# Kernel tuning notes

Hardware: AMD Instinct MI355X
Metric: run time of the kernel (lower is better)

Reference implementation:

```python
import jax, jax.numpy as jnp
import numpy as np

EPS = 1e-12  # torch F.normalize eps


def _pairwise_unit_diffs(x):
    # x: [B, N, D] -> unit-normalized pairwise diffs [B, N*N, D]
    B, N, D = x.shape
    d = x[:, :, None, :] - x[:, None, :, :]            # [B, N, N, D]
    n = jnp.linalg.norm(d, axis=-1, keepdims=True)
    d = d / jnp.maximum(n, EPS)                        # zero rows stay zero
    return d.reshape(B, N * N, D)


def setup_inputs() -> dict:
    key = jax.random.key(0)
    k1, k2 = jax.random.split(key)
    B, N, D = 4, 64, 128
    student = jax.random.normal(k1, (B, N, D), dtype=jnp.float32)
    teacher = jax.random.normal(k2, (B, N, D), dtype=jnp.float32)
    return {"student": student, "teacher": teacher}


def reference(student, teacher):
    B, N, D = student.shape
    sd = _pairwise_unit_diffs(student)                              # [B, N^2, D]
    td = jax.lax.stop_gradient(_pairwise_unit_diffs(teacher))      # [B, N^2, D]
    s_ang = jnp.einsum('bkd,bld->bkl', sd, sd)
    t_ang = jax.lax.stop_gradient(jnp.einsum('bkd,bld->bkl', td, td))
    # smooth L1 (beta=1.0), summed then divided by total element count
    diff = s_ang - t_ang
    ad = jnp.abs(diff)
    loss = jnp.where(ad < 1.0, 0.5 * diff * diff, ad - 0.5)
    count = B * (N * N) * (N * N)
    return jnp.sum(loss) / count
```

## Files before the change

### kernel.cpp

```cpp
#include <hip/hip_runtime.h>


#define EPSF 1e-12f

typedef __bf16 bf16x8 __attribute__((ext_vector_type(8)));
typedef float  f32x4  __attribute__((ext_vector_type(4)));

__device__ __forceinline__ float rinv_from_nsq(float nsq)
{
    float n = sqrtf(fmaxf(nsq, 0.0f));
    return 1.0f / fmaxf(n, EPSF);
}

__device__ __forceinline__ void cvt8(float4 u, float4 v, bf16x8& h, bf16x8& l)
{
    float uu[8] = {u.x, u.y, u.z, u.w, v.x, v.y, v.z, v.w};
#pragma unroll
    for (int i = 0; i < 8; ++i) {
        __bf16 hh = (__bf16)uu[i];
        h[i] = hh;
        l[i] = (__bf16)(uu[i] - (float)hh);
    }
}

__global__ __launch_bounds__(512) void fused_kernel(
    const float* __restrict__ student, const float* __restrict__ teacher,
    float* __restrict__ out)
{
    __shared__ float Gs[4096];
    __shared__ float Gt[4096];
    __shared__ __align__(16) float pool[17408];
    __shared__ float red[8];

    int b   = blockIdx.x / 63;
    int kc  = blockIdx.x % 63;
    int tid = threadIdx.x;

    {
        int r  = tid >> 3;
        int f8 = tid & 7;
        const float* Xs = student + b * 8192 + r * 128 + f8 * 16;
        const float* Xt = teacher + b * 8192 + r * 128 + f8 * 16;
        float* sHi = pool + 0 * 4352 + r * 68 + f8 * 8;
        float* sLo = pool + 1 * 4352 + r * 68 + f8 * 8;
        float* tHi = pool + 2 * 4352 + r * 68 + f8 * 8;
        float* tLo = pool + 3 * 4352 + r * 68 + f8 * 8;
#pragma unroll
        for (int c = 0; c < 2; ++c) {
            float4 u = *(const float4*)(Xs + c * 8);
            float4 v = *(const float4*)(Xs + c * 8 + 4);
            bf16x8 h, l;
            cvt8(u, v, h, l);
            *(bf16x8*)(sHi + c * 4) = h;
            *(bf16x8*)(sLo + c * 4) = l;
            u = *(const float4*)(Xt + c * 8);
            v = *(const float4*)(Xt + c * 8 + 4);
            cvt8(u, v, h, l);
            *(bf16x8*)(tHi + c * 4) = h;
            *(bf16x8*)(tLo + c * 4) = l;
        }
    }
    __syncthreads();

    {
        int wid  = tid >> 6;
        int lane = tid & 63;
        int l15  = lane & 15;
        int quad = lane >> 4;
        int tensor = wid >> 2;
        int mt     = wid & 3;
        const float* XH = pool + tensor * 8704;
        const float* XL = XH + 4352;

        bf16x8 aH[4], aL[4];
        int abase = (mt * 16 + l15) * 68 + quad * 4;
#pragma unroll
        for (int ks = 0; ks < 4; ++ks) {
            aH[ks] = *(const bf16x8*)(XH + abase + ks * 16);
            aL[ks] = *(const bf16x8*)(XL + abase + ks * 16);
        }
        float* Gd = tensor ? Gt : Gs;
#pragma unroll
        for (int nt = 0; nt < 4; ++nt) {
            f32x4 acc = {0.f, 0.f, 0.f, 0.f};
            int bbase = (nt * 16 + l15) * 68 + quad * 4;
#pragma unroll
            for (int ks = 0; ks < 4; ++ks) {
                bf16x8 bH = *(const bf16x8*)(XH + bbase + ks * 16);
                bf16x8 bL = *(const bf16x8*)(XL + bbase + ks * 16);
                acc = __builtin_amdgcn_mfma_f32_16x16x32_bf16(aH[ks], bH, acc, 0, 0, 0);
                acc = __builtin_amdgcn_mfma_f32_16x16x32_bf16(aH[ks], bL, acc, 0, 0, 0);
                acc = __builtin_amdgcn_mfma_f32_16x16x32_bf16(aL[ks], bH, acc, 0, 0, 0);
                acc = __builtin_amdgcn_mfma_f32_16x16x32_bf16(aL[ks], bL, acc, 0, 0, 0);
            }
#pragma unroll
            for (int reg = 0; reg < 4; ++reg)
                Gd[(mt * 16 + quad * 4 + reg) * 64 + nt * 16 + l15] = acc[reg];
        }
    }
    __syncthreads();

    float* vs = pool;
    float* vt = pool + 2176;

    {
        int m  = tid >> 4;
        int q4 = (tid & 15) * 4;
        int t  = kc * 32 + m;
        int i = 0, rem = t;
        while (rem >= 63 - i) { rem -= 63 - i; ++i; }
        int j = i + 1 + rem;

        float rsij = rinv_from_nsq(Gs[i * 65] - 2.f * Gs[i * 64 + j] + Gs[j * 65]);
        float rtij = rinv_from_nsq(Gt[i * 65] - 2.f * Gt[i * 64 + j] + Gt[j * 65]);

        float4 gis = *(const float4*)(Gs + i * 64 + q4);
        float4 gjs = *(const float4*)(Gs + j * 64 + q4);
        float4 git = *(const float4*)(Gt + i * 64 + q4);
        float4 gjt = *(const float4*)(Gt + j * 64 + q4);
        float4 v;
        v.x = (gis.x - gjs.x) * rsij;
        v.y = (gis.y - gjs.y) * rsij;
        v.z = (gis.z - gjs.z) * rsij;
        v.w = (gis.w - gjs.w) * rsij;
        *(float4*)(vs + m * 68 + q4) = v;
        v.x = (git.x - gjt.x) * rtij;
        v.y = (git.y - gjt.y) * rtij;
        v.z = (git.z - gjt.z) * rtij;
        v.w = (git.w - gjt.w) * rtij;
        *(float4*)(vt + m * 68 + q4) = v;
    }

    int msub = tid >> 7;
    int pos  = tid & 127;
    int pg = 0, qg = 0;
    float4 rsv[4], rtv[4];
    if (pos < 120) {
        int rem = pos;
        while (rem >= 15 - pg) { rem -= 15 - pg; ++pg; }
        qg = pg + 1 + rem;
        int p4  = pg * 4;
        float dps[4], dpt[4];
#pragma unroll
        for (int cc = 0; cc < 4; ++cc) {
            dps[cc] = Gs[(p4 + cc) * 65];
            dpt[cc] = Gt[(p4 + cc) * 65];
        }
#pragma unroll
        for (int k = 0; k < 4; ++k) {
            int q = qg * 4 + k;
            float4 g = *(const float4*)(Gs + q * 64 + p4);
            float gqq = Gs[q * 65];
            rsv[k].x = rinv_from_nsq(dps[0] - 2.f * g.x + gqq);
            rsv[k].y = rinv_from_nsq(dps[1] - 2.f * g.y + gqq);
            rsv[k].z = rinv_from_nsq(dps[2] - 2.f * g.z + gqq);
            rsv[k].w = rinv_from_nsq(dps[3] - 2.f * g.w + gqq);
            float4 hh = *(const float4*)(Gt + q * 64 + p4);
            float hqq = Gt[q * 65];
            rtv[k].x = rinv_from_nsq(dpt[0] - 2.f * hh.x + hqq);
            rtv[k].y = rinv_from_nsq(dpt[1] - 2.f * hh.y + hqq);
            rtv[k].z = rinv_from_nsq(dpt[2] - 2.f * hh.z + hqq);
            rtv[k].w = rinv_from_nsq(dpt[3] - 2.f * hh.w + hqq);
        }
    }
    __syncthreads();

    float ac0 = 0.f, ac1 = 0.f, ac2 = 0.f, ac3 = 0.f;

#define SL1(acc, spc, sqc, tpc, tqc, rsk, rtk)                                  \
    {                                                                           \
        float d  = (spc - sqc) * rsk - (tpc - tqc) * rtk;                       \
        float a  = fabsf(d);                                                    \
        float mn = fminf(a, 1.0f);                                              \
        acc = fmaf(mn, fmaf(-0.5f, mn, a), acc);                                \
    }

    if (pos < 120) {
        int p4  = pg * 4;
        int q4l = qg * 4;
#pragma unroll 4
        for (int mm = 0; mm < 8; ++mm) {
            int m = mm * 4 + msub;
            const float* vsm = vs + m * 68;
            const float* vtm = vt + m * 68;
            float4 sp = *(const float4*)(vsm + p4);
            float4 tp = *(const float4*)(vtm + p4);
            float4 sq = *(const float4*)(vsm + q4l);
            float4 tq = *(const float4*)(vtm + q4l);

            SL1(ac0, sp.x, sq.x, tp.x, tq.x, rsv[0].x, rtv[0].x)
            SL1(ac0, sp.y, sq.x, tp.y, tq.x, rsv[0].y, rtv[0].y)
            SL1(ac0, sp.z, sq.x, tp.z, tq.x, rsv[0].z, rtv[0].z)
            SL1(ac0, sp.w, sq.x, tp.w, tq.x, rsv[0].w, rtv[0].w)

            SL1(ac1, sp.x, sq.y, tp.x, tq.y, rsv[1].x, rtv[1].x)
            SL1(ac1, sp.y, sq.y, tp.y, tq.y, rsv[1].y, rtv[1].y)
            SL1(ac1, sp.z, sq.y, tp.z, tq.y, rsv[1].z, rtv[1].z)
            SL1(ac1, sp.w, sq.y, tp.w, tq.y, rsv[1].w, rtv[1].w)

            SL1(ac2, sp.x, sq.z, tp.x, tq.z, rsv[2].x, rtv[2].x)
            SL1(ac2, sp.y, sq.z, tp.y, tq.z, rsv[2].y, rtv[2].y)
            SL1(ac2, sp.z, sq.z, tp.z, tq.z, rsv[2].z, rtv[2].z)
            SL1(ac2, sp.w, sq.z, tp.w, tq.z, rsv[2].w, rtv[2].w)

            SL1(ac3, sp.x, sq.w, tp.x, tq.w, rsv[3].x, rtv[3].x)
            SL1(ac3, sp.y, sq.w, tp.y, tq.w, rsv[3].y, rtv[3].y)
            SL1(ac3, sp.z, sq.w, tp.z, tq.w, rsv[3].z, rtv[3].z)
            SL1(ac3, sp.w, sq.w, tp.w, tq.w, rsv[3].w, rtv[3].w)
        }
    }

    {
        int m  = tid >> 4;
        int g4 = (tid & 15) * 4;
        float4 s4 = *(const float4*)(vs + m * 68 + g4);
        float4 t4 = *(const float4*)(vt + m * 68 + g4);

        float d0s = Gs[(g4 + 0) * 65], d1s = Gs[(g4 + 1) * 65];
        float d2s = Gs[(g4 + 2) * 65], d3s = Gs[(g4 + 3) * 65];
        float d0t = Gt[(g4 + 0) * 65], d1t = Gt[(g4 + 1) * 65];
        float d2t = Gt[(g4 + 2) * 65], d3t = Gt[(g4 + 3) * 65];

        float rs01 = rinv_from_nsq(d0s - 2.f * Gs[(g4 + 0) * 64 + g4 + 1] + d1s);
        float rs02 = rinv_from_nsq(d0s - 2.f * Gs[(g4 + 0) * 64 + g4 + 2] + d2s);
        float rs03 = rinv_from_nsq(d0s - 2.f * Gs[(g4 + 0) * 64 + g4 + 3] + d3s);
        float rs12 = rinv_from_nsq(d1s - 2.f * Gs[(g4 + 1) * 64 + g4 + 2] + d2s);
        float rs13 = rinv_from_nsq(d1s - 2.f * Gs[(g4 + 1) * 64 + g4 + 3] + d3s);
        float rs23 = rinv_from_nsq(d2s - 2.f * Gs[(g4 + 2) * 64 + g4 + 3] + d3s);
        float rt01 = rinv_from_nsq(d0t - 2.f * Gt[(g4 + 0) * 64 + g4 + 1] + d1t);
        float rt02 = rinv_from_nsq(d0t - 2.f * Gt[(g4 + 0) * 64 + g4 + 2] + d2t);
        float rt03 = rinv_from_nsq(d0t - 2.f * Gt[(g4 + 0) * 64 + g4 + 3] + d3t);
        float rt12 = rinv_from_nsq(d1t - 2.f * Gt[(g4 + 1) * 64 + g4 + 2] + d2t);
        float rt13 = rinv_from_nsq(d1t - 2.f * Gt[(g4 + 1) * 64 + g4 + 3] + d3t);
        float rt23 = rinv_from_nsq(d2t - 2.f * Gt[(g4 + 2) * 64 + g4 + 3] + d3t);

        SL1(ac0, s4.x, s4.y, t4.x, t4.y, rs01, rt01)
        SL1(ac1, s4.x, s4.z, t4.x, t4.z, rs02, rt02)
        SL1(ac2, s4.x, s4.w, t4.x, t4.w, rs03, rt03)
        SL1(ac3, s4.y, s4.z, t4.y, t4.z, rs12, rt12)
        SL1(ac0, s4.y, s4.w, t4.y, t4.w, rs13, rt13)
        SL1(ac1, s4.z, s4.w, t4.z, t4.w, rs23, rt23)
    }
#undef SL1

    float acc = (ac0 + ac1) + (ac2 + ac3);

    for (int off = 32; off > 0; off >>= 1)
        acc += __shfl_down(acc, off);
    int lane = tid & 63;
    int wave = tid >> 6;
    if (lane == 0) red[wave] = acc;
    __syncthreads();
    if (tid < 8) {
        float v = red[tid];
        v += __shfl_down(v, 4);
        v += __shfl_down(v, 2);
        v += __shfl_down(v, 1);
        if (tid == 0) atomicAdd(out, v * (1.0f / 16777216.0f));
    }
}

extern "C" void kernel_launch(void* const* d_in, const int* in_sizes, int n_in,
                              void* d_out, int out_size, void* d_ws, size_t ws_size,
                              hipStream_t stream)
{
    const float* student = (const float*)d_in[0];
    const float* teacher = (const float*)d_in[1];
    (void)d_ws; (void)ws_size;
    fused_kernel<<<252, 512, 0, stream>>>(student, teacher, (float*)d_out);
}
```

Baseline: 68.91 us.

## Double block size, precompute inverse pair norms table in LDS, closed-form pair indexing

Raises the block to 1024 threads and spreads every phase (load/convert, MFMA Gram, vector build, SL1 loop) across twice as many waves. Adds a shared-memory table of reciprocal pairwise distance norms, built once with the hardware rsq instruction, so the later stages read it instead of recomputing sqrt and divide many times. Replaces the serial while-loops that map a linear index to a triangular (i,j) pair with a closed-form sqrt formula plus a correction step. The gain in parallelism comes with an extra barrier, heavier register pressure under the 1024-thread launch bound, and slightly different rounding from rsq.

```diff
diff --git a/kernel.cpp b/kernel.cpp
--- a/kernel.cpp
+++ b/kernel.cpp
@@ -1,15 +1,14 @@
 #include <hip/hip_runtime.h>
 
 
-#define EPSF 1e-12f
+#define EPSQ 1e-24f
 
 typedef __bf16 bf16x8 __attribute__((ext_vector_type(8)));
 typedef float  f32x4  __attribute__((ext_vector_type(4)));
 
-__device__ __forceinline__ float rinv_from_nsq(float nsq)
-{
-    float n = sqrtf(fmaxf(nsq, 0.0f));
-    return 1.0f / fmaxf(n, EPSF);
+__device__ __forceinline__ float rinv_nsq(float nsq)
+{
+    return __builtin_amdgcn_rsqf(fmaxf(nsq, EPSQ));
 }
 
 __device__ __forceinline__ void cvt8(float4 u, float4 v, bf16x8& h, bf16x8& l)
@@ -23,42 +22,39 @@
     }
 }
 
-__global__ __launch_bounds__(512) void fused_kernel(
+__global__ __launch_bounds__(1024) void fused_kernel(
     const float* __restrict__ student, const float* __restrict__ teacher,
     float* __restrict__ out)
 {
     __shared__ float Gs[4096];
     __shared__ float Gt[4096];
     __shared__ __align__(16) float pool[17408];
-    __shared__ float red[8];
+    __shared__ float red[16];
 
     int b   = blockIdx.x / 63;
     int kc  = blockIdx.x % 63;
     int tid = threadIdx.x;
 
     {
-        int r  = tid >> 3;
-        int f8 = tid & 7;
-        const float* Xs = student + b * 8192 + r * 128 + f8 * 16;
-        const float* Xt = teacher + b * 8192 + r * 128 + f8 * 16;
-        float* sHi = pool + 0 * 4352 + r * 68 + f8 * 8;
-        float* sLo = pool + 1 * 4352 + r * 68 + f8 * 8;
-        float* tHi = pool + 2 * 4352 + r * 68 + f8 * 8;
-        float* tLo = pool + 3 * 4352 + r * 68 + f8 * 8;
-#pragma unroll
-        for (int c = 0; c < 2; ++c) {
-            float4 u = *(const float4*)(Xs + c * 8);
-            float4 v = *(const float4*)(Xs + c * 8 + 4);
-            bf16x8 h, l;
-            cvt8(u, v, h, l);
-            *(bf16x8*)(sHi + c * 4) = h;
-            *(bf16x8*)(sLo + c * 4) = l;
-            u = *(const float4*)(Xt + c * 8);
-            v = *(const float4*)(Xt + c * 8 + 4);
-            cvt8(u, v, h, l);
-            *(bf16x8*)(tHi + c * 4) = h;
-            *(bf16x8*)(tLo + c * 4) = l;
-        }
+        int r = tid >> 4;
+        int h = tid & 15;
+        const float* Xs = student + b * 8192 + r * 128 + h * 8;
+        const float* Xt = teacher + b * 8192 + r * 128 + h * 8;
+        float* sHi = pool + 0 * 4352 + r * 68 + h * 4;
+        float* sLo = pool + 1 * 4352 + r * 68 + h * 4;
+        float* tHi = pool + 2 * 4352 + r * 68 + h * 4;
+        float* tLo = pool + 3 * 4352 + r * 68 + h * 4;
+        float4 u = *(const float4*)(Xs);
+        float4 v = *(const float4*)(Xs + 4);
+        bf16x8 hh, ll;
+        cvt8(u, v, hh, ll);
+        *(bf16x8*)sHi = hh;
+        *(bf16x8*)sLo = ll;
+        u = *(const float4*)(Xt);
+        v = *(const float4*)(Xt + 4);
+        cvt8(u, v, hh, ll);
+        *(bf16x8*)tHi = hh;
+        *(bf16x8*)tLo = ll;
     }
     __syncthreads();
 
@@ -67,8 +63,10 @@
         int lane = tid & 63;
         int l15  = lane & 15;
         int quad = lane >> 4;
-        int tensor = wid >> 2;
-        int mt     = wid & 3;
+        int tensor = wid >> 3;
+        int w8     = wid & 7;
+        int mt     = w8 >> 1;
+        int nh     = w8 & 1;
         const float* XH = pool + tensor * 8704;
         const float* XL = XH + 4352;
 
@@ -81,7 +79,8 @@
         }
         float* Gd = tensor ? Gt : Gs;
 #pragma unroll
-        for (int nt = 0; nt < 4; ++nt) {
+        for (int nn = 0; nn < 2; ++nn) {
+            int nt = nh * 2 + nn;
             f32x4 acc = {0.f, 0.f, 0.f, 0.f};
             int bbase = (nt * 16 + l15) * 68 + quad * 4;
 #pragma unroll
@@ -100,35 +99,58 @@
     }
     __syncthreads();
 
-    float* vs = pool;
-    float* vt = pool + 2176;
-
-    {
-        int m  = tid >> 4;
-        int q4 = (tid & 15) * 4;
+    float* vs  = pool;
+    float* vt  = pool + 2176;
+    float* rnS = pool + 4352;
+    float* rnT = pool + 8448;
+
+    {
+        int tensor = tid >> 9;
+        int u      = tid & 511;
+        int p      = u >> 3;
+        int q0     = (u & 7) * 8;
+        const float* Gd = tensor ? Gt : Gs;
+        float*       rn = tensor ? rnT : rnS;
+        float dp = Gd[p * 65];
+        float4 g0 = *(const float4*)(Gd + p * 64 + q0);
+        float4 g1 = *(const float4*)(Gd + p * 64 + q0 + 4);
+        float4 o0, o1;
+        o0.x = rinv_nsq(dp - 2.f * g0.x + Gd[(q0 + 0) * 65]);
+        o0.y = rinv_nsq(dp - 2.f * g0.y + Gd[(q0 + 1) * 65]);
+        o0.z = rinv_nsq(dp - 2.f * g0.z + Gd[(q0 + 2) * 65]);
+        o0.w = rinv_nsq(dp - 2.f * g0.w + Gd[(q0 + 3) * 65]);
+        o1.x = rinv_nsq(dp - 2.f * g1.x + Gd[(q0 + 4) * 65]);
+        o1.y = rinv_nsq(dp - 2.f * g1.y + Gd[(q0 + 5) * 65]);
+        o1.z = rinv_nsq(dp - 2.f * g1.z + Gd[(q0 + 6) * 65]);
+        o1.w = rinv_nsq(dp - 2.f * g1.w + Gd[(q0 + 7) * 65]);
+        *(float4*)(rn + p * 64 + q0)     = o0;
+        *(float4*)(rn + p * 64 + q0 + 4) = o1;
+    }
+    __syncthreads();
+
+    {
+        int m  = tid >> 5;
+        int qh = (tid & 31) * 2;
         int t  = kc * 32 + m;
-        int i = 0, rem = t;
-        while (rem >= 63 - i) { rem -= 63 - i; ++i; }
-        int j = i + 1 + rem;
-
-        float rsij = rinv_from_nsq(Gs[i * 65] - 2.f * Gs[i * 64 + j] + Gs[j * 65]);
-        float rtij = rinv_from_nsq(Gt[i * 65] - 2.f * Gt[i * 64 + j] + Gt[j * 65]);
-
-        float4 gis = *(const float4*)(Gs + i * 64 + q4);
-        float4 gjs = *(const float4*)(Gs + j * 64 + q4);
-        float4 git = *(const float4*)(Gt + i * 64 + q4);
-        float4 gjt = *(const float4*)(Gt + j * 64 + q4);
-        float4 v;
-        v.x = (gis.x - gjs.x) * rsij;
-        v.y = (gis.y - gjs.y) * rsij;
-        v.z = (gis.z - gjs.z) * rsij;
-        v.w = (gis.w - gjs.w) * rsij;
-        *(float4*)(vs + m * 68 + q4) = v;
-        v.x = (git.x - gjt.x) * rtij;
-        v.y = (git.y - gjt.y) * rtij;
-        v.z = (git.z - gjt.z) * rtij;
-        v.w = (git.w - gjt.w) * rtij;
-        *(float4*)(vt + m * 68 + q4) = v;
+        int i = (int)(0.5f * (127.0f - sqrtf((float)(16129 - 8 * t))));
+        if (i * (127 - i) / 2 > t) --i;
+        else if ((i + 1) * (126 - i) / 2 <= t) ++i;
+        int j = i + 1 + (t - i * (127 - i) / 2);
+
+        float rsij = rnS[i * 64 + j];
+        float rtij = rnT[i * 64 + j];
+
+        float2 gi = *(const float2*)(Gs + i * 64 + qh);
+        float2 gj = *(const float2*)(Gs + j * 64 + qh);
+        float2 o;
+        o.x = (gi.x - gj.x) * rsij;
+        o.y = (gi.y - gj.y) * rsij;
+        *(float2*)(vs + m * 68 + qh) = o;
+        gi = *(const float2*)(Gt + i * 64 + qh);
+        gj = *(const float2*)(Gt + j * 64 + qh);
+        o.x = (gi.x - gj.x) * rtij;
+        o.y = (gi.y - gj.y) * rtij;
+        *(float2*)(vt + m * 68 + qh) = o;
     }
 
     int msub = tid >> 7;
@@ -136,31 +158,15 @@
     int pg = 0, qg = 0;
     float4 rsv[4], rtv[4];
     if (pos < 120) {
-        int rem = pos;
-        while (rem >= 15 - pg) { rem -= 15 - pg; ++pg; }
-        qg = pg + 1 + rem;
-        int p4  = pg * 4;
-        float dps[4], dpt[4];
-#pragma unroll
-        for (int cc = 0; cc < 4; ++cc) {
-            dps[cc] = Gs[(p4 + cc) * 65];
-            dpt[cc] = Gt[(p4 + cc) * 65];
-        }
+        pg = (int)(0.5f * (31.0f - sqrtf((float)(961 - 8 * pos))));
+        if (pg * (31 - pg) / 2 > pos) --pg;
+        else if ((pg + 1) * (30 - pg) / 2 <= pos) ++pg;
+        qg = pg + 1 + (pos - pg * (31 - pg) / 2);
+        int p4 = pg * 4;
 #pragma unroll
         for (int k = 0; k < 4; ++k) {
-            int q = qg * 4 + k;
-            float4 g = *(const float4*)(Gs + q * 64 + p4);
-            float gqq = Gs[q * 65];
-            rsv[k].x = rinv_from_nsq(dps[0] - 2.f * g.x + gqq);
-            rsv[k].y = rinv_from_nsq(dps[1] - 2.f * g.y + gqq);
-            rsv[k].z = rinv_from_nsq(dps[2] - 2.f * g.z + gqq);
-            rsv[k].w = rinv_from_nsq(dps[3] - 2.f * g.w + gqq);
-            float4 hh = *(const float4*)(Gt + q * 64 + p4);
-            float hqq = Gt[q * 65];
-            rtv[k].x = rinv_from_nsq(dpt[0] - 2.f * hh.x + hqq);
-            rtv[k].y = rinv_from_nsq(dpt[1] - 2.f * hh.y + hqq);
-            rtv[k].z = rinv_from_nsq(dpt[2] - 2.f * hh.z + hqq);
-            rtv[k].w = rinv_from_nsq(dpt[3] - 2.f * hh.w + hqq);
+            rsv[k] = *(const float4*)(rnS + (qg * 4 + k) * 64 + p4);
+            rtv[k] = *(const float4*)(rnT + (qg * 4 + k) * 64 + p4);
         }
     }
     __syncthreads();
@@ -178,9 +184,9 @@
     if (pos < 120) {
         int p4  = pg * 4;
         int q4l = qg * 4;
-#pragma unroll 4
-        for (int mm = 0; mm < 8; ++mm) {
-            int m = mm * 4 + msub;
+#pragma unroll
+        for (int mm = 0; mm < 4; ++mm) {
+            int m = mm * 8 + msub;
             const float* vsm = vs + m * 68;
             const float* vtm = vt + m * 68;
             float4 sp = *(const float4*)(vsm + p4);
@@ -210,29 +216,24 @@
         }
     }
 
-    {
+    if (tid < 512) {
         int m  = tid >> 4;
         int g4 = (tid & 15) * 4;
         float4 s4 = *(const float4*)(vs + m * 68 + g4);
         float4 t4 = *(const float4*)(vt + m * 68 + g4);
 
-        float d0s = Gs[(g4 + 0) * 65], d1s = Gs[(g4 + 1) * 65];
-        float d2s = Gs[(g4 + 2) * 65], d3s = Gs[(g4 + 3) * 65];
-        float d0t = Gt[(g4 + 0) * 65], d1t = Gt[(g4 + 1) * 65];
-        float d2t = Gt[(g4 + 2) * 65], d3t = Gt[(g4 + 3) * 65];
-
-        float rs01 = rinv_from_nsq(d0s - 2.f * Gs[(g4 + 0) * 64 + g4 + 1] + d1s);
-        float rs02 = rinv_from_nsq(d0s - 2.f * Gs[(g4 + 0) * 64 + g4 + 2] + d2s);
-        float rs03 = rinv_from_nsq(d0s - 2.f * Gs[(g4 + 0) * 64 + g4 + 3] + d3s);
-        float rs12 = rinv_from_nsq(d1s - 2.f * Gs[(g4 + 1) * 64 + g4 + 2] + d2s);
-        float rs13 = rinv_from_nsq(d1s - 2.f * Gs[(g4 + 1) * 64 + g4 + 3] + d3s);
-        float rs23 = rinv_from_nsq(d2s - 2.f * Gs[(g4 + 2) * 64 + g4 + 3] + d3s);
-        float rt01 = rinv_from_nsq(d0t - 2.f * Gt[(g4 + 0) * 64 + g4 + 1] + d1t);
-        float rt02 = rinv_from_nsq(d0t - 2.f * Gt[(g4 + 0) * 64 + g4 + 2] + d2t);
-        float rt03 = rinv_from_nsq(d0t - 2.f * Gt[(g4 + 0) * 64 + g4 + 3] + d3t);
-        float rt12 = rinv_from_nsq(d1t - 2.f * Gt[(g4 + 1) * 64 + g4 + 2] + d2t);
-        float rt13 = rinv_from_nsq(d1t - 2.f * Gt[(g4 + 1) * 64 + g4 + 3] + d3t);
-        float rt23 = rinv_from_nsq(d2t - 2.f * Gt[(g4 + 2) * 64 + g4 + 3] + d3t);
+        float rs01 = rnS[(g4 + 0) * 64 + g4 + 1];
+        float rs02 = rnS[(g4 + 0) * 64 + g4 + 2];
+        float rs03 = rnS[(g4 + 0) * 64 + g4 + 3];
+        float rs12 = rnS[(g4 + 1) * 64 + g4 + 2];
+        float rs13 = rnS[(g4 + 1) * 64 + g4 + 3];
+        float rs23 = rnS[(g4 + 2) * 64 + g4 + 3];
+        float rt01 = rnT[(g4 + 0) * 64 + g4 + 1];
+        float rt02 = rnT[(g4 + 0) * 64 + g4 + 2];
+        float rt03 = rnT[(g4 + 0) * 64 + g4 + 3];
+        float rt12 = rnT[(g4 + 1) * 64 + g4 + 2];
+        float rt13 = rnT[(g4 + 1) * 64 + g4 + 3];
+        float rt23 = rnT[(g4 + 2) * 64 + g4 + 3];
 
         SL1(ac0, s4.x, s4.y, t4.x, t4.y, rs01, rt01)
         SL1(ac1, s4.x, s4.z, t4.x, t4.z, rs02, rt02)
@@ -251,8 +252,9 @@
     int wave = tid >> 6;
     if (lane == 0) red[wave] = acc;
     __syncthreads();
-    if (tid < 8) {
+    if (tid < 16) {
         float v = red[tid];
+        v += __shfl_down(v, 8);
         v += __shfl_down(v, 4);
         v += __shfl_down(v, 2);
         v += __shfl_down(v, 1);
@@ -267,5 +269,5 @@
     const float* student = (const float*)d_in[0];
     const float* teacher = (const float*)d_in[1];
     (void)d_ws; (void)ws_size;
-    fused_kernel<<<252, 512, 0, stream>>>(student, teacher, (float*)d_out);
-}
+    fused_kernel<<<252, 1024, 0, stream>>>(student, teacher, (float*)d_out);
+}
```

Result: faster. 66.03 us (-4.2%).
